# Kernel tuning notes

Hardware: AMD Instinct MI355X
Metric: run time of the kernel (lower is better)

Reference implementation:

```python
import jax, jax.numpy as jnp
from jax import lax
import numpy as np

N_SEQ, BATCH, HID = 512, 32, 1024

def setup_inputs() -> dict:
    key = jax.random.key(0)
    k1, k2, k3 = jax.random.split(key, 3)
    Y = jax.random.normal(k1, (N_SEQ, BATCH, 3 * HID), dtype=jnp.float32)
    init_c = jax.random.normal(k2, (1, BATCH, HID), dtype=jnp.float32)
    init_h = jax.random.normal(k3, (1, BATCH, HID), dtype=jnp.float32)
    return {"Y": Y, "init_c": init_c, "init_h": init_h}

def reference(Y, init_c, init_h):
    # QRNN fo-pooling: c_t = f_t * c_{t-1} + (1 - f_t) * z_t ; h_t = o_t * c_t
    # Zoneout dropout is evaluated in inference mode (identity), so F is used as-is.
    F, Z, O = jnp.split(Y, 3, axis=2)       # each [T, B, H]
    F = jax.nn.sigmoid(F)
    Z = jnp.tanh(Z)
    O = jax.nn.sigmoid(O)
    ZF = (1.0 - F) * Z

    def step(c, inp):
        f, zf, o = inp
        c = f * c + zf
        return c, c * o

    _, h = lax.scan(step, init_c[0], (F, ZF, O))  # h: [T, B, H]
    return jnp.concatenate([init_h, h], axis=0)   # [T+1, B, H]
```

## Files before the change

kernel.cpp:

```cpp
#include <hip/hip_runtime.h>


#define T_SEQ 512
#define BATCH 32
#define HID   1024
#define CH    (BATCH * HID)
#define CH4   (CH / 4)
#define HID4  (HID / 4)
#define ROWS4 (BATCH * 3 * HID4)
#define NC    128
#define CL    (T_SEQ / NC)
#define JW    8
#define NTHR  (NC * JW)

__device__ __forceinline__ float fast_sigmoid(float x) {
    float e = __builtin_amdgcn_exp2f(-1.4426950408889634f * x);
    return __builtin_amdgcn_rcpf(1.0f + e);
}
__device__ __forceinline__ float fast_tanh(float x) {
    float e = __builtin_amdgcn_exp2f(-2.8853900817779268f * x);
    float s = __builtin_amdgcn_rcpf(1.0f + e);
    return __builtin_fmaf(2.0f, s, -1.0f);
}
__device__ __forceinline__ float4 sig4(float4 v) {
    return make_float4(fast_sigmoid(v.x), fast_sigmoid(v.y),
                       fast_sigmoid(v.z), fast_sigmoid(v.w));
}
__device__ __forceinline__ float4 fma4(float4 a, float4 b, float4 c) {
    return make_float4(__builtin_fmaf(a.x, b.x, c.x), __builtin_fmaf(a.y, b.y, c.y),
                       __builtin_fmaf(a.z, b.z, c.z), __builtin_fmaf(a.w, b.w, c.w));
}

__global__ __launch_bounds__(NTHR) void fo_pool_fused(
        const float4* __restrict__ Y4,
        const float4* __restrict__ init_c4,
        const float4* __restrict__ init_h4,
        float4* __restrict__ out4) {
    __shared__ float4 sA[NC][JW];
    __shared__ float4 sB[NC][JW];

    const int tid = threadIdx.x;
    const int k   = tid >> 3;
    const int j   = tid & (JW - 1);
    const int c4  = blockIdx.x * JW + j;
    const int b   = c4 >> 8;
    const int h4  = c4 & (HID4 - 1);
    const float4* yb = Y4 + b * (3 * HID4) + h4 + (size_t)(k * CL) * ROWS4;

    float4 fr[CL], zr[CL];
#pragma unroll
    for (int t = 0; t < CL; ++t) {
        const float4* p = yb + (size_t)t * ROWS4;
        fr[t] = p[0]; zr[t] = p[HID4];
    }
    float4 ff[CL], gg[CL];
    float4 A  = make_float4(1.f, 1.f, 1.f, 1.f);
    float4 Bv = make_float4(0.f, 0.f, 0.f, 0.f);
#pragma unroll
    for (int t = 0; t < CL; ++t) {
        float4 s = sig4(fr[t]);
        float4 g;
        g.x = (1.f - s.x) * fast_tanh(zr[t].x);
        g.y = (1.f - s.y) * fast_tanh(zr[t].y);
        g.z = (1.f - s.z) * fast_tanh(zr[t].z);
        g.w = (1.f - s.w) * fast_tanh(zr[t].w);
        ff[t] = s; gg[t] = g;
        Bv = fma4(s, Bv, g);
        A.x *= s.x; A.y *= s.y; A.z *= s.z; A.w *= s.w;
    }
    sA[k][j] = A;
    sB[k][j] = Bv;
    __syncthreads();

#pragma unroll
    for (int d = 1; d < NC; d <<= 1) {
        float4 pa, pb;
        const bool has = (k >= d);
        if (has) { pa = sA[k - d][j]; pb = sB[k - d][j]; }
        __syncthreads();
        if (has) {
            float4 a  = sA[k][j];
            float4 bb = sB[k][j];
            sA[k][j] = make_float4(a.x * pa.x, a.y * pa.y, a.z * pa.z, a.w * pa.w);
            sB[k][j] = fma4(a, pb, bb);
        }
        __syncthreads();
    }

    const float4 c0 = init_c4[c4];
    float4 c;
    if (k == 0) {
        c = c0;
        out4[c4] = init_h4[c4];
    } else {
        c = fma4(sA[k - 1][j], c0, sB[k - 1][j]);
    }

    float4 orr[CL];
#pragma unroll
    for (int t = 0; t < CL; ++t) orr[t] = (yb + (size_t)t * ROWS4)[2 * HID4];

    float4* ob = out4 + (size_t)(k * CL + 1) * CH4 + c4;
#pragma unroll
    for (int t = 0; t < CL; ++t) {
        c = fma4(ff[t], c, gg[t]);
        float4 oo = sig4(orr[t]);
        ob[(size_t)t * CH4] = make_float4(c.x * oo.x, c.y * oo.y, c.z * oo.z, c.w * oo.w);
    }
}

extern "C" void kernel_launch(void* const* d_in, const int* in_sizes, int n_in,
                              void* d_out, int out_size, void* d_ws, size_t ws_size,
                              hipStream_t stream) {
    const float* Y      = (const float*)d_in[0];
    const float* init_c = (const float*)d_in[1];
    const float* init_h = (const float*)d_in[2];
    float* out = (float*)d_out;

    fo_pool_fused<<<CH4 / JW, NTHR, 0, stream>>>(
        (const float4*)Y, (const float4*)init_c, (const float4*)init_h, (float4*)out);
}
```

Before: 312.0 us.

## Replace shared-memory Hillis-Steele scan with wave shuffle scan plus per-wave carry

```diff
diff --git a/kernel.cpp b/kernel.cpp
--- a/kernel.cpp
+++ b/kernel.cpp
@@ -12,6 +12,7 @@
 #define CL    (T_SEQ / NC)
 #define JW    8
 #define NTHR  (NC * JW)
+#define NWAVE (NTHR / 64)
 
 __device__ __forceinline__ float fast_sigmoid(float x) {
     float e = __builtin_amdgcn_exp2f(-1.4426950408889634f * x);
@@ -30,29 +31,40 @@
     return make_float4(__builtin_fmaf(a.x, b.x, c.x), __builtin_fmaf(a.y, b.y, c.y),
                        __builtin_fmaf(a.z, b.z, c.z), __builtin_fmaf(a.w, b.w, c.w));
 }
+__device__ __forceinline__ float4 mul4(float4 a, float4 b) {
+    return make_float4(a.x * b.x, a.y * b.y, a.z * b.z, a.w * b.w);
+}
+__device__ __forceinline__ float4 shflup4(float4 v, int delta) {
+    return make_float4(__shfl_up(v.x, delta, 64), __shfl_up(v.y, delta, 64),
+                       __shfl_up(v.z, delta, 64), __shfl_up(v.w, delta, 64));
+}
 
 __global__ __launch_bounds__(NTHR) void fo_pool_fused(
         const float4* __restrict__ Y4,
         const float4* __restrict__ init_c4,
         const float4* __restrict__ init_h4,
         float4* __restrict__ out4) {
-    __shared__ float4 sA[NC][JW];
-    __shared__ float4 sB[NC][JW];
+    __shared__ float4 sWA[NWAVE][JW];
+    __shared__ float4 sWB[NWAVE][JW];
 
     const int tid = threadIdx.x;
+    const int j   = tid & (JW - 1);
     const int k   = tid >> 3;
-    const int j   = tid & (JW - 1);
+    const int kl  = k & 7;
+    const int w   = tid >> 6;
     const int c4  = blockIdx.x * JW + j;
     const int b   = c4 >> 8;
     const int h4  = c4 & (HID4 - 1);
     const float4* yb = Y4 + b * (3 * HID4) + h4 + (size_t)(k * CL) * ROWS4;
 
-    float4 fr[CL], zr[CL];
+    float4 fr[CL], zr[CL], orr[CL];
 #pragma unroll
     for (int t = 0; t < CL; ++t) {
         const float4* p = yb + (size_t)t * ROWS4;
-        fr[t] = p[0]; zr[t] = p[HID4];
+        fr[t] = p[0]; zr[t] = p[HID4]; orr[t] = p[2 * HID4];
     }
+    const float4 c0 = init_c4[c4];
+
     float4 ff[CL], gg[CL];
     float4 A  = make_float4(1.f, 1.f, 1.f, 1.f);
     float4 Bv = make_float4(0.f, 0.f, 0.f, 0.f);
@@ -66,46 +78,47 @@
         g.w = (1.f - s.w) * fast_tanh(zr[t].w);
         ff[t] = s; gg[t] = g;
         Bv = fma4(s, Bv, g);
-        A.x *= s.x; A.y *= s.y; A.z *= s.z; A.w *= s.w;
+        A  = mul4(A, s);
     }
-    sA[k][j] = A;
-    sB[k][j] = Bv;
+
+#pragma unroll
+    for (int d = 1; d < 8; d <<= 1) {
+        float4 pa = shflup4(A, 8 * d);
+        float4 pb = shflup4(Bv, 8 * d);
+        if (kl >= d) {
+            Bv = fma4(A, pb, Bv);
+            A  = mul4(A, pa);
+        }
+    }
+
+    if (kl == 7) { sWA[w][j] = A; sWB[w][j] = Bv; }
+    __syncthreads();
+    if (tid < JW) {
+        float4 RA = make_float4(1.f, 1.f, 1.f, 1.f);
+        float4 RB = make_float4(0.f, 0.f, 0.f, 0.f);
+#pragma unroll
+        for (int ww = 0; ww < NWAVE; ++ww) {
+            float4 ta = sWA[ww][tid], tb = sWB[ww][tid];
+            sWA[ww][tid] = RA; sWB[ww][tid] = RB;
+            RB = fma4(ta, RB, tb);
+            RA = mul4(ta, RA);
+        }
+    }
     __syncthreads();
 
-#pragma unroll
-    for (int d = 1; d < NC; d <<= 1) {
-        float4 pa, pb;
-        const bool has = (k >= d);
-        if (has) { pa = sA[k - d][j]; pb = sB[k - d][j]; }
-        __syncthreads();
-        if (has) {
-            float4 a  = sA[k][j];
-            float4 bb = sB[k][j];
-            sA[k][j] = make_float4(a.x * pa.x, a.y * pa.y, a.z * pa.z, a.w * pa.w);
-            sB[k][j] = fma4(a, pb, bb);
-        }
-        __syncthreads();
-    }
+    float4 cpre = fma4(sWA[w][j], c0, sWB[w][j]);
+    float4 qa = shflup4(A, 8), qb = shflup4(Bv, 8);
+    float4 c  = (kl == 0) ? cpre : fma4(qa, cpre, qb);
 
-    const float4 c0 = init_c4[c4];
-    float4 c;
-    if (k == 0) {
-        c = c0;
-        out4[c4] = init_h4[c4];
-    } else {
-        c = fma4(sA[k - 1][j], c0, sB[k - 1][j]);
-    }
-
-    float4 orr[CL];
-#pragma unroll
-    for (int t = 0; t < CL; ++t) orr[t] = (yb + (size_t)t * ROWS4)[2 * HID4];
+    if (k == 0) out4[c4] = init_h4[c4];
 
     float4* ob = out4 + (size_t)(k * CL + 1) * CH4 + c4;
 #pragma unroll
     for (int t = 0; t < CL; ++t) {
         c = fma4(ff[t], c, gg[t]);
         float4 oo = sig4(orr[t]);
-        ob[(size_t)t * CH4] = make_float4(c.x * oo.x, c.y * oo.y, c.z * oo.z, c.w * oo.w);
+        ob[(size_t)t * CH4] = make_float4(c.x * oo.x, c.y * oo.y,
+                                          c.z * oo.z, c.w * oo.w);
     }
 }
 
```

Measured after the change: 307.5 us. No clear change (-1.4%).
